# Kernel optimization log

Measured on AMD Instinct MI355X. Metric: run time of the kernel, lower is better.

## Reference

```python
import jax, jax.numpy as jnp
import numpy as np

B, T_ENC, T_DEC = 8, 1024, 100
DMODEL, H, DK, DV, DFF = 512, 8, 64, 64, 2048
L_ENC, L_DEC = 2, 2
EPS = 1e-5
MASK_FILL = -1e10  # original code masked_fills the post-softmax probs with -1e10


def _ln(x, g, b):
    m = jnp.mean(x, -1, keepdims=True)
    v = jnp.mean(jnp.square(x - m), -1, keepdims=True)
    return (x - m) * jax.lax.rsqrt(v + EPS) * g + b


def _mha(Q, K, V, Wq, Wk, Wv, causal):
    Bz, Lq, _ = Q.shape
    Lk = K.shape[1]
    q = (Q @ Wq).reshape(Bz, Lq, H, DK).transpose(0, 2, 1, 3)  # b h q d
    k = (K @ Wk).reshape(Bz, Lk, H, DK).transpose(0, 2, 1, 3)
    v = (V @ Wv).reshape(Bz, Lk, H, DV).transpose(0, 2, 1, 3)
    scores = jnp.einsum('bhqd,bhkd->bhqk', q, k) * (1.0 / np.float32(np.sqrt(DK)))
    p = jax.nn.softmax(scores, axis=-1)
    if causal:
        # faithful to original: mask applied AFTER softmax, fill value -1e10
        mask = jnp.tril(jnp.ones((Lq, Lk), dtype=bool))
        p = jnp.where(mask[None, None], p, jnp.float32(MASK_FILL))
    o = jnp.einsum('bhqk,bhkd->bhqd', p, v)
    return o.transpose(0, 2, 1, 3).reshape(Bz, Lq, H * DV)


def setup_inputs() -> dict:
    key = jax.random.key(0)
    ks = iter(jax.random.split(key, 64))
    s = 0.02
    d = {
        'x': jax.random.normal(next(ks), (B, T_ENC, DMODEL), jnp.float32),
        'y': jax.random.normal(next(ks), (B, T_DEC, DMODEL), jnp.float32),
    }
    def w(shape):
        return jax.random.normal(next(ks), shape, jnp.float32) * s
    # encoder params, stacked over layers
    d['enc_Wq'] = w((L_ENC, DMODEL, DMODEL)); d['enc_Wk'] = w((L_ENC, DMODEL, H * DK))
    d['enc_Wv'] = w((L_ENC, DMODEL, H * DV))
    d['enc_ff_w1'] = w((L_ENC, DMODEL, DFF)); d['enc_ff_b1'] = jnp.zeros((L_ENC, DFF))
    d['enc_ff_w2'] = w((L_ENC, DFF, DMODEL)); d['enc_ff_b2'] = jnp.zeros((L_ENC, DMODEL))
    d['enc_ln1_g'] = jnp.ones((L_ENC, DMODEL)); d['enc_ln1_b'] = jnp.zeros((L_ENC, DMODEL))
    d['enc_ln2_g'] = jnp.ones((L_ENC, DMODEL)); d['enc_ln2_b'] = jnp.zeros((L_ENC, DMODEL))
    # decoder params
    d['dec_Wq1'] = w((L_DEC, DMODEL, DMODEL)); d['dec_Wk1'] = w((L_DEC, DMODEL, H * DK))
    d['dec_Wv1'] = w((L_DEC, DMODEL, H * DV))
    d['dec_Wq2'] = w((L_DEC, DMODEL, DMODEL)); d['dec_Wk2'] = w((L_DEC, DMODEL, H * DK))
    d['dec_Wv2'] = w((L_DEC, DMODEL, H * DV))
    d['dec_ff_w1'] = w((L_DEC, DMODEL, DFF)); d['dec_ff_b1'] = jnp.zeros((L_DEC, DFF))
    d['dec_ff_w2'] = w((L_DEC, DFF, DMODEL)); d['dec_ff_b2'] = jnp.zeros((L_DEC, DMODEL))
    d['dec_ln1_g'] = jnp.ones((L_DEC, DMODEL)); d['dec_ln1_b'] = jnp.zeros((L_DEC, DMODEL))
    d['dec_ln2_g'] = jnp.ones((L_DEC, DMODEL)); d['dec_ln2_b'] = jnp.zeros((L_DEC, DMODEL))
    d['dec_ln3_g'] = jnp.ones((L_DEC, DMODEL)); d['dec_ln3_b'] = jnp.zeros((L_DEC, DMODEL))
    return d


def reference(x, y,
              enc_Wq, enc_Wk, enc_Wv, enc_ff_w1, enc_ff_b1, enc_ff_w2, enc_ff_b2,
              enc_ln1_g, enc_ln1_b, enc_ln2_g, enc_ln2_b,
              dec_Wq1, dec_Wk1, dec_Wv1, dec_Wq2, dec_Wk2, dec_Wv2,
              dec_ff_w1, dec_ff_b1, dec_ff_w2, dec_ff_b2,
              dec_ln1_g, dec_ln1_b, dec_ln2_g, dec_ln2_b, dec_ln3_g, dec_ln3_b):
    # encoder stacks
    for i in range(L_ENC):
        att = _mha(x, x, x, enc_Wq[i], enc_Wk[i], enc_Wv[i], causal=False)
        x1 = _ln(x + att, enc_ln1_g[i], enc_ln1_b[i])
        ff = jax.nn.relu(x1 @ enc_ff_w1[i] + enc_ff_b1[i]) @ enc_ff_w2[i] + enc_ff_b2[i]
        x = _ln(x1 + ff, enc_ln2_g[i], enc_ln2_b[i])
    # decoder stacks
    for i in range(L_DEC):
        a1 = _mha(y, y, y, dec_Wq1[i], dec_Wk1[i], dec_Wv1[i], causal=True)
        y1 = _ln(y + a1, dec_ln1_g[i], dec_ln1_b[i])
        a2 = _mha(y1, x, x, dec_Wq2[i], dec_Wk2[i], dec_Wv2[i], causal=False)
        y2 = _ln(y1 + a2, dec_ln2_g[i], dec_ln2_b[i])
        ff = jax.nn.relu(y2 @ dec_ff_w1[i] + dec_ff_b1[i]) @ dec_ff_w2[i] + dec_ff_b2[i]
        y = _ln(y2 + ff, dec_ln3_g[i], dec_ln3_b[i])
    return y
```

## Files before the change

kernel.cpp:

```cpp
#include <hip/hip_runtime.h>
#include <cstddef>

typedef unsigned short u16;
typedef __attribute__((ext_vector_type(8))) short bf16x8;
typedef __attribute__((ext_vector_type(4))) float f32x4;

__device__ __forceinline__ u16 f2b(float f) {
    union { float f; unsigned u; } x; x.f = f;
    unsigned r = x.u + 0x7FFFu + ((x.u >> 16) & 1u);
    return (u16)(r >> 16);
}
__device__ __forceinline__ float b2f(u16 v) {
    union { unsigned u; float f; } x; x.u = ((unsigned)v) << 16;
    return x.f;
}

__device__ __forceinline__ void gload_lds16(const u16* g, u16* l) {
    __builtin_amdgcn_global_load_lds(
        (const __attribute__((address_space(1))) void*)g,
        (__attribute__((address_space(3))) void*)l, 16, 0, 0);
}

__global__ __launch_bounds__(256) void gemm_mfma_kernel(
    const u16* __restrict__ A, const u16* __restrict__ Bt,
    const float* __restrict__ bias,
    float* __restrict__ Cf, u16* __restrict__ Cb,
    int M, int K, int N, int relu)
{
    __shared__ __align__(16) u16 As[2][128 * 32];
    __shared__ __align__(16) u16 Bs[2][128 * 32];

    const int tid  = threadIdx.x;
    const int wave = tid >> 6;
    const int lane = tid & 63;
    const int m0 = blockIdx.y * 128;
    const int n0 = blockIdx.x * 128;

    const int wm = (wave & 1) * 64;
    const int wn = (wave >> 1) * 64;

    const int srow  = lane >> 2;
    const int skoff = (lane & 3) * 8;

    const int r0 = wave * 32;
    int gr0 = m0 + r0 + srow;       if (gr0 >= M) gr0 = M - 1;
    int gr1 = m0 + r0 + 16 + srow;  if (gr1 >= M) gr1 = M - 1;
    const u16* a0 = A + (size_t)gr0 * K + skoff;
    const u16* a1 = A + (size_t)gr1 * K + skoff;
    const u16* b0p = Bt + (size_t)(n0 + r0 + srow) * K + skoff;
    const u16* b1p = Bt + (size_t)(n0 + r0 + 16 + srow) * K + skoff;

    f32x4 acc[4][4];
#pragma unroll
    for (int i = 0; i < 4; ++i)
#pragma unroll
        for (int j = 0; j < 4; ++j)
            acc[i][j] = (f32x4){0.f, 0.f, 0.f, 0.f};

    const int fm = lane & 15;
    const int fk = (lane >> 4) * 8;

    const int NK = K >> 5;

    gload_lds16(a0, &As[0][(r0) * 32]);
    gload_lds16(a1, &As[0][(r0 + 16) * 32]);
    gload_lds16(b0p, &Bs[0][(r0) * 32]);
    gload_lds16(b1p, &Bs[0][(r0 + 16) * 32]);

    for (int t = 0; t < NK; ++t) {
        const int cur = t & 1;
        __asm__ volatile("s_waitcnt lgkmcnt(0)" ::: "memory");
        __builtin_amdgcn_s_barrier();
        if (t + 1 < NK) {
            const int nxt = (t + 1) & 1;
            const int ko = (t + 1) << 5;
            gload_lds16(a0 + ko, &As[nxt][(r0) * 32]);
            gload_lds16(a1 + ko, &As[nxt][(r0 + 16) * 32]);
            gload_lds16(b0p + ko, &Bs[nxt][(r0) * 32]);
            gload_lds16(b1p + ko, &Bs[nxt][(r0 + 16) * 32]);
            __asm__ volatile("s_waitcnt vmcnt(4)" ::: "memory");
        } else {
            __asm__ volatile("s_waitcnt vmcnt(0)" ::: "memory");
        }
        __builtin_amdgcn_s_barrier();

        bf16x8 af[4], bfr[4];
#pragma unroll
        for (int u = 0; u < 4; ++u) {
            af[u]  = *(const bf16x8*)(&As[cur][(wm + u * 16 + fm) * 32 + fk]);
            bfr[u] = *(const bf16x8*)(&Bs[cur][(wn + u * 16 + fm) * 32 + fk]);
        }
#pragma unroll
        for (int i = 0; i < 4; ++i)
#pragma unroll
            for (int j = 0; j < 4; ++j)
                acc[i][j] = __builtin_amdgcn_mfma_f32_16x16x32_bf16(
                    af[i], bfr[j], acc[i][j], 0, 0, 0);
    }

    const int col = lane & 15;
    const int rq  = (lane >> 4) * 4;
#pragma unroll
    for (int j = 0; j < 4; ++j) {
        const int gn = n0 + wn + j * 16 + col;
        const float bb = bias ? bias[gn] : 0.f;
#pragma unroll
        for (int i = 0; i < 4; ++i) {
            const int gmb = m0 + wm + i * 16 + rq;
#pragma unroll
            for (int r = 0; r < 4; ++r) {
                const int gm = gmb + r;
                if (gm < M) {
                    float v = acc[i][j][r] + bb;
                    if (relu) v = fmaxf(v, 0.f);
                    if (Cb) Cb[(size_t)gm * N + gn] = f2b(v);
                    else    Cf[(size_t)gm * N + gn] = v;
                }
            }
        }
    }
}

__global__ __launch_bounds__(256) void gemm64_kernel(
    const u16* __restrict__ A, const u16* __restrict__ Bt,
    const float* __restrict__ bias,
    float* __restrict__ Cf, u16* __restrict__ Cb,
    int M, int K, int N, int relu)
{
    __shared__ __align__(16) u16 As[2][64 * 32];
    __shared__ __align__(16) u16 Bs[2][64 * 32];

    const int tid  = threadIdx.x;
    const int wave = tid >> 6;
    const int lane = tid & 63;
    const int m0 = blockIdx.y * 64;
    const int n0 = blockIdx.x * 64;
    const int wm = (wave & 1) * 32;
    const int wn = (wave >> 1) * 32;

    const int srow  = lane >> 2;
    const int skoff = (lane & 3) * 8;

    int gr = m0 + wave * 16 + srow; if (gr >= M) gr = M - 1;
    const u16* ap = A + (size_t)gr * K + skoff;
    const u16* bp = Bt + (size_t)(n0 + wave * 16 + srow) * K + skoff;

    f32x4 acc[2][2];
#pragma unroll
    for (int i = 0; i < 2; ++i)
#pragma unroll
        for (int j = 0; j < 2; ++j) acc[i][j] = (f32x4){0.f, 0.f, 0.f, 0.f};

    const int fm = lane & 15;
    const int fk = (lane >> 4) * 8;

    const int NK = K >> 5;

    gload_lds16(ap, &As[0][(wave * 16) * 32]);
    gload_lds16(bp, &Bs[0][(wave * 16) * 32]);

    for (int t = 0; t < NK; ++t) {
        const int cur = t & 1;
        __asm__ volatile("s_waitcnt lgkmcnt(0)" ::: "memory");
        __builtin_amdgcn_s_barrier();
        if (t + 1 < NK) {
            const int nxt = (t + 1) & 1;
            const int ko = (t + 1) << 5;
            gload_lds16(ap + ko, &As[nxt][(wave * 16) * 32]);
            gload_lds16(bp + ko, &Bs[nxt][(wave * 16) * 32]);
            __asm__ volatile("s_waitcnt vmcnt(2)" ::: "memory");
        } else {
            __asm__ volatile("s_waitcnt vmcnt(0)" ::: "memory");
        }
        __builtin_amdgcn_s_barrier();

        bf16x8 af[2], bfr[2];
#pragma unroll
        for (int u = 0; u < 2; ++u) {
            af[u]  = *(const bf16x8*)(&As[cur][(wm + u * 16 + fm) * 32 + fk]);
            bfr[u] = *(const bf16x8*)(&Bs[cur][(wn + u * 16 + fm) * 32 + fk]);
        }
#pragma unroll
        for (int i = 0; i < 2; ++i)
#pragma unroll
            for (int j = 0; j < 2; ++j)
                acc[i][j] = __builtin_amdgcn_mfma_f32_16x16x32_bf16(
                    af[i], bfr[j], acc[i][j], 0, 0, 0);
    }

    const int col = lane & 15;
    const int rq  = (lane >> 4) * 4;
#pragma unroll
    for (int j = 0; j < 2; ++j) {
        const int gn = n0 + wn + j * 16 + col;
        const float bb = bias ? bias[gn] : 0.f;
#pragma unroll
        for (int i = 0; i < 2; ++i) {
            const int gmb = m0 + wm + i * 16 + rq;
#pragma unroll
            for (int r = 0; r < 4; ++r) {
                const int gm = gmb + r;
                if (gm < M) {
                    float v = acc[i][j][r] + bb;
                    if (relu) v = fmaxf(v, 0.f);
                    if (Cb) Cb[(size_t)gm * N + gn] = f2b(v);
                    else    Cf[(size_t)gm * N + gn] = v;
                }
            }
        }
    }
}

__global__ __launch_bounds__(256) void attn_mfma_kernel(
    const u16* __restrict__ Qp, const u16* __restrict__ Kp,
    const u16* __restrict__ Vp, u16* __restrict__ Op,
    int Lq, int Lk, int ldq, int ldkv, int ldo)
{
    const int q0 = blockIdx.x * 128;
    const int h  = blockIdx.y;
    const int b  = blockIdx.z;
    const int tid  = threadIdx.x;
    const int wave = tid >> 6;
    const int lane = tid & 63;
    const int c = lane & 15;
    const int g = lane >> 4;
    const float scale = 0.125f;

    __shared__ __align__(16) u16 Ks[128 * 72];
    __shared__ __align__(16) u16 Vs[64 * 144];
    __shared__ __align__(16) u16 Ps[128 * 144];

    bf16x8 aq[2][2];
#pragma unroll
    for (int half = 0; half < 2; ++half) {
        int qrow = q0 + wave * 32 + half * 16 + c;
        if (qrow > Lq - 1) qrow = Lq - 1;
        const u16* src = Qp + ((size_t)(b * Lq + qrow)) * ldq + h * 64 + g * 8;
        aq[half][0] = *(const bf16x8*)(src);
        aq[half][1] = *(const bf16x8*)(src + 32);
    }

    float den[2][4] = {};
    f32x4 o[2][4];
#pragma unroll
    for (int half = 0; half < 2; ++half)
#pragma unroll
        for (int j = 0; j < 4; ++j) o[half][j] = (f32x4){0.f, 0.f, 0.f, 0.f};

    const int srow = tid & 63;
    const int sseg = tid >> 6;

    for (int t = 0; t < (Lk >> 7); ++t) {
        const int k0 = t << 7;
        __syncthreads();
#pragma unroll
        for (int sub = 0; sub < 2; ++sub) {
            const int kr = k0 + sub * 64 + srow;
            const u16* kg = Kp + ((size_t)(b * Lk + kr)) * ldkv + h * 64;
            *(bf16x8*)(&Ks[(sub * 64 + srow) * 72 + sseg * 8])      = *(const bf16x8*)(kg + sseg * 8);
            *(bf16x8*)(&Ks[(sub * 64 + srow) * 72 + 32 + sseg * 8]) = *(const bf16x8*)(kg + 32 + sseg * 8);
            const u16* vg = Vp + ((size_t)(b * Lk + kr)) * ldkv + h * 64;
            bf16x8 v0 = *(const bf16x8*)(vg + sseg * 8);
            bf16x8 v1 = *(const bf16x8*)(vg + 32 + sseg * 8);
#pragma unroll
            for (int i = 0; i < 8; ++i) {
                Vs[(sseg * 8 + i) * 144 + sub * 64 + srow]      = (u16)v0[i];
                Vs[(32 + sseg * 8 + i) * 144 + sub * 64 + srow] = (u16)v1[i];
            }
        }
        __syncthreads();

#pragma unroll
        for (int half = 0; half < 2; ++half) {
            f32x4 s[8];
#pragma unroll
            for (int jn = 0; jn < 8; ++jn) s[jn] = (f32x4){0.f, 0.f, 0.f, 0.f};
#pragma unroll
            for (int jn = 0; jn < 8; ++jn) {
                bf16x8 b0 = *(const bf16x8*)(&Ks[(jn * 16 + c) * 72 + g * 8]);
                bf16x8 b1 = *(const bf16x8*)(&Ks[(jn * 16 + c) * 72 + 32 + g * 8]);
                s[jn] = __builtin_amdgcn_mfma_f32_16x16x32_bf16(aq[half][0], b0, s[jn], 0, 0, 0);
                s[jn] = __builtin_amdgcn_mfma_f32_16x16x32_bf16(aq[half][1], b1, s[jn], 0, 0, 0);
            }
#pragma unroll
            for (int jn = 0; jn < 8; ++jn)
#pragma unroll
                for (int r = 0; r < 4; ++r) {
                    const float p = __expf(s[jn][r] * scale);
                    den[half][r] += p;
                    Ps[(wave * 32 + half * 16 + g * 4 + r) * 144 + jn * 16 + c] = f2b(p);
                }
        }

        __asm__ volatile("s_waitcnt lgkmcnt(0)" ::: "memory");

#pragma unroll
        for (int half = 0; half < 2; ++half) {
            const int qr = (wave * 32 + half * 16 + c) * 144;
#pragma unroll
            for (int sub = 0; sub < 2; ++sub) {
                bf16x8 ap0 = *(const bf16x8*)(&Ps[qr + sub * 64 + g * 8]);
                bf16x8 ap1 = *(const bf16x8*)(&Ps[qr + sub * 64 + 32 + g * 8]);
#pragma unroll
                for (int jd = 0; jd < 4; ++jd) {
                    bf16x8 b0 = *(const bf16x8*)(&Vs[(jd * 16 + c) * 144 + sub * 64 + g * 8]);
                    bf16x8 b1 = *(const bf16x8*)(&Vs[(jd * 16 + c) * 144 + sub * 64 + 32 + g * 8]);
                    o[half][jd] = __builtin_amdgcn_mfma_f32_16x16x32_bf16(ap0, b0, o[half][jd], 0, 0, 0);
                    o[half][jd] = __builtin_amdgcn_mfma_f32_16x16x32_bf16(ap1, b1, o[half][jd], 0, 0, 0);
                }
            }
        }
    }

#pragma unroll
    for (int half = 0; half < 2; ++half)
#pragma unroll
        for (int r = 0; r < 4; ++r) {
#pragma unroll
            for (int msk = 1; msk < 16; msk <<= 1)
                den[half][r] += __shfl_xor(den[half][r], msk, 64);
        }

#pragma unroll
    for (int half = 0; half < 2; ++half)
#pragma unroll
        for (int r = 0; r < 4; ++r) {
            const int q = q0 + wave * 32 + half * 16 + g * 4 + r;
            if (q < Lq) {
                const float inv = 1.0f / den[half][r];
#pragma unroll
                for (int jd = 0; jd < 4; ++jd)
                    Op[((size_t)(b * Lq + q)) * ldo + h * 64 + jd * 16 + c] =
                        f2b(o[half][jd][r] * inv);
            }
        }
}

__global__ __launch_bounds__(256) void attn_causal_kernel(
    const u16* __restrict__ Qp, const u16* __restrict__ Kp,
    const u16* __restrict__ Vp, const float* __restrict__ SuffV,
    u16* __restrict__ Op,
    int Lq, int Lk, int ldq, int ldkv, int ldo)
{
    const int q0 = blockIdx.x * 128;
    const int h  = blockIdx.y;
    const int b  = blockIdx.z;
    const int tid  = threadIdx.x;
    const int wave = tid >> 6;
    const int lane = tid & 63;
    const int c = lane & 15;
    const int g = lane >> 4;
    const float scale = 0.125f;

    __shared__ __align__(16) u16 Ks[64 * 72];
    __shared__ __align__(16) u16 Vs[64 * 72];
    __shared__ __align__(16) u16 Ps[128 * 72];

    bf16x8 aq[2][2];
#pragma unroll
    for (int half = 0; half < 2; ++half) {
        int qrow = q0 + wave * 32 + half * 16 + c;
        if (qrow > Lq - 1) qrow = Lq - 1;
        const u16* src = Qp + ((size_t)(b * Lq + qrow)) * ldq + h * 64 + g * 8;
        aq[half][0] = *(const bf16x8*)(src);
        aq[half][1] = *(const bf16x8*)(src + 32);
    }

    float den[2][4] = {};
    f32x4 o[2][4];
#pragma unroll
    for (int half = 0; half < 2; ++half)
#pragma unroll
        for (int j = 0; j < 4; ++j) o[half][j] = (f32x4){0.f, 0.f, 0.f, 0.f};

    const int srow = tid & 63;
    const int sseg = tid >> 6;
    const int ntiles = (Lk + 63) >> 6;

    for (int t = 0; t < ntiles; ++t) {
        const int k0 = t << 6;
        __syncthreads();
        {
            int kr = k0 + srow; if (kr > Lk - 1) kr = Lk - 1;
            const u16* kg = Kp + ((size_t)(b * Lk + kr)) * ldkv + h * 64;
            *(bf16x8*)(&Ks[srow * 72 + sseg * 8])      = *(const bf16x8*)(kg + sseg * 8);
            *(bf16x8*)(&Ks[srow * 72 + 32 + sseg * 8]) = *(const bf16x8*)(kg + 32 + sseg * 8);
            const u16* vg = Vp + ((size_t)(b * Lk + kr)) * ldkv + h * 64;
            bf16x8 v0 = *(const bf16x8*)(vg + sseg * 8);
            bf16x8 v1 = *(const bf16x8*)(vg + 32 + sseg * 8);
#pragma unroll
            for (int i = 0; i < 8; ++i) {
                Vs[(sseg * 8 + i) * 72 + srow]      = (u16)v0[i];
                Vs[(32 + sseg * 8 + i) * 72 + srow] = (u16)v1[i];
            }
        }
        __syncthreads();

#pragma unroll
        for (int half = 0; half < 2; ++half) {
            f32x4 s[4];
#pragma unroll
            for (int jn = 0; jn < 4; ++jn) s[jn] = (f32x4){0.f, 0.f, 0.f, 0.f};
#pragma unroll
            for (int jn = 0; jn < 4; ++jn) {
                bf16x8 b0 = *(const bf16x8*)(&Ks[(jn * 16 + c) * 72 + g * 8]);
                bf16x8 b1 = *(const bf16x8*)(&Ks[(jn * 16 + c) * 72 + 32 + g * 8]);
                s[jn] = __builtin_amdgcn_mfma_f32_16x16x32_bf16(aq[half][0], b0, s[jn], 0, 0, 0);
                s[jn] = __builtin_amdgcn_mfma_f32_16x16x32_bf16(aq[half][1], b1, s[jn], 0, 0, 0);
            }
#pragma unroll
            for (int jn = 0; jn < 4; ++jn)
#pragma unroll
                for (int r = 0; r < 4; ++r) {
                    const int kcol = k0 + jn * 16 + c;
                    const int qrow = q0 + wave * 32 + half * 16 + g * 4 + r;
                    const float e = __expf(s[jn][r] * scale);
                    const float ev = (kcol < Lk) ? e : 0.f;
                    den[half][r] += ev;
                    const float pv = (kcol <= qrow) ? ev : 0.f;
                    Ps[(wave * 32 + half * 16 + g * 4 + r) * 72 + jn * 16 + c] = f2b(pv);
                }
        }

        __asm__ volatile("s_waitcnt lgkmcnt(0)" ::: "memory");

#pragma unroll
        for (int half = 0; half < 2; ++half) {
            bf16x8 ap0 = *(const bf16x8*)(&Ps[(wave * 32 + half * 16 + c) * 72 + g * 8]);
            bf16x8 ap1 = *(const bf16x8*)(&Ps[(wave * 32 + half * 16 + c) * 72 + 32 + g * 8]);
#pragma unroll
            for (int jd = 0; jd < 4; ++jd) {
                bf16x8 b0 = *(const bf16x8*)(&Vs[(jd * 16 + c) * 72 + g * 8]);
                bf16x8 b1 = *(const bf16x8*)(&Vs[(jd * 16 + c) * 72 + 32 + g * 8]);
                o[half][jd] = __builtin_amdgcn_mfma_f32_16x16x32_bf16(ap0, b0, o[half][jd], 0, 0, 0);
                o[half][jd] = __builtin_amdgcn_mfma_f32_16x16x32_bf16(ap1, b1, o[half][jd], 0, 0, 0);
            }
        }
    }

#pragma unroll
    for (int half = 0; half < 2; ++half)
#pragma unroll
        for (int r = 0; r < 4; ++r) {
#pragma unroll
            for (int msk = 1; msk < 16; msk <<= 1)
                den[half][r] += __shfl_xor(den[half][r], msk, 64);
        }

#pragma unroll
    for (int half = 0; half < 2; ++half)
#pragma unroll
        for (int r = 0; r < 4; ++r) {
            const int q = q0 + wave * 32 + half * 16 + g * 4 + r;
            if (q < Lq) {
                const float inv = 1.0f / den[half][r];
                const float* sv = SuffV + ((size_t)(b * Lq + q)) * 512 + h * 64;
#pragma unroll
                for (int jd = 0; jd < 4; ++jd)
                    Op[((size_t)(b * Lq + q)) * ldo + h * 64 + jd * 16 + c] =
                        f2b(o[half][jd][r] * inv - 1.0e10f * sv[jd * 16 + c]);
            }
        }
}

__global__ __launch_bounds__(64) void suffv_kernel(
    const u16* __restrict__ Vp, float* __restrict__ SuffV, int Lq, int ldv)
{
    const int b = blockIdx.x;
    const int h = blockIdx.y;
    const int d = threadIdx.x;
    float acc = 0.f;
    for (int q = Lq - 1; q >= 0; --q) {
        SuffV[((size_t)(b * Lq + q)) * 512 + h * 64 + d] = acc;
        acc += b2f(Vp[((size_t)(b * Lq + q)) * ldv + h * 64 + d]);
    }
}

__global__ __launch_bounds__(256) void attn_split_kernel(
    const u16* __restrict__ Qp, const u16* __restrict__ Kp,
    const u16* __restrict__ Vp, float* __restrict__ Opart,
    float* __restrict__ Dpart,
    int Lq, int Lk, int ldq, int ldkv, int nsplit)
{
    const int q0 = blockIdx.x * 64;
    const int h  = blockIdx.y;
    const int b  = blockIdx.z / nsplit;
    const int sp = blockIdx.z % nsplit;
    const int tid  = threadIdx.x;
    const int wave = tid >> 6;
    const int lane = tid & 63;
    const int c = lane & 15;
    const int g = lane >> 4;
    const float scale = 0.125f;
    const int rowsTot = gridDim.z / nsplit * Lq;

    __shared__ __align__(16) u16 Ks[64 * 72];
    __shared__ __align__(16) u16 Vs[64 * 72];
    __shared__ __align__(16) u16 Ps[64 * 72];

    bf16x8 aq[2];
    {
        int qrow = q0 + wave * 16 + c;
        if (qrow > Lq - 1) qrow = Lq - 1;
        const u16* src = Qp + ((size_t)(b * Lq + qrow)) * ldq + h * 64 + g * 8;
        aq[0] = *(const bf16x8*)(src);
        aq[1] = *(const bf16x8*)(src + 32);
    }

    float den[4] = {0.f, 0.f, 0.f, 0.f};
    f32x4 o[4];
#pragma unroll
    for (int j = 0; j < 4; ++j) o[j] = (f32x4){0.f, 0.f, 0.f, 0.f};

    const int srow = tid & 63;
    const int sseg = tid >> 6;
    const int ntile = (Lk >> 6) / nsplit;

    for (int t = sp * ntile; t < (sp + 1) * ntile; ++t) {
        const int k0 = t << 6;
        __syncthreads();
        {
            const u16* kg = Kp + ((size_t)(b * Lk + k0 + srow)) * ldkv + h * 64;
            *(bf16x8*)(&Ks[srow * 72 + sseg * 8])      = *(const bf16x8*)(kg + sseg * 8);
            *(bf16x8*)(&Ks[srow * 72 + 32 + sseg * 8]) = *(const bf16x8*)(kg + 32 + sseg * 8);
            const u16* vg = Vp + ((size_t)(b * Lk + k0 + srow)) * ldkv + h * 64;
            bf16x8 v0 = *(const bf16x8*)(vg + sseg * 8);
            bf16x8 v1 = *(const bf16x8*)(vg + 32 + sseg * 8);
#pragma unroll
            for (int i = 0; i < 8; ++i) {
                Vs[(sseg * 8 + i) * 72 + srow]      = (u16)v0[i];
                Vs[(32 + sseg * 8 + i) * 72 + srow] = (u16)v1[i];
            }
        }
        __syncthreads();

        f32x4 s[4];
#pragma unroll
        for (int jn = 0; jn < 4; ++jn) s[jn] = (f32x4){0.f, 0.f, 0.f, 0.f};
#pragma unroll
        for (int jn = 0; jn < 4; ++jn) {
            bf16x8 b0 = *(const bf16x8*)(&Ks[(jn * 16 + c) * 72 + g * 8]);
            bf16x8 b1 = *(const bf16x8*)(&Ks[(jn * 16 + c) * 72 + 32 + g * 8]);
            s[jn] = __builtin_amdgcn_mfma_f32_16x16x32_bf16(aq[0], b0, s[jn], 0, 0, 0);
            s[jn] = __builtin_amdgcn_mfma_f32_16x16x32_bf16(aq[1], b1, s[jn], 0, 0, 0);
        }
#pragma unroll
        for (int jn = 0; jn < 4; ++jn)
#pragma unroll
            for (int r = 0; r < 4; ++r) {
                const float p = __expf(s[jn][r] * scale);
                den[r] += p;
                Ps[(wave * 16 + g * 4 + r) * 72 + jn * 16 + c] = f2b(p);
            }

        __asm__ volatile("s_waitcnt lgkmcnt(0)" ::: "memory");

        bf16x8 ap0 = *(const bf16x8*)(&Ps[(wave * 16 + c) * 72 + g * 8]);
        bf16x8 ap1 = *(const bf16x8*)(&Ps[(wave * 16 + c) * 72 + 32 + g * 8]);
#pragma unroll
        for (int jd = 0; jd < 4; ++jd) {
            bf16x8 b0 = *(const bf16x8*)(&Vs[(jd * 16 + c) * 72 + g * 8]);
            bf16x8 b1 = *(const bf16x8*)(&Vs[(jd * 16 + c) * 72 + 32 + g * 8]);
            o[jd] = __builtin_amdgcn_mfma_f32_16x16x32_bf16(ap0, b0, o[jd], 0, 0, 0);
            o[jd] = __builtin_amdgcn_mfma_f32_16x16x32_bf16(ap1, b1, o[jd], 0, 0, 0);
        }
    }

#pragma unroll
    for (int r = 0; r < 4; ++r) {
#pragma unroll
        for (int msk = 1; msk < 16; msk <<= 1)
            den[r] += __shfl_xor(den[r], msk, 64);
    }

#pragma unroll
    for (int r = 0; r < 4; ++r) {
        const int q = q0 + wave * 16 + g * 4 + r;
        if (q < Lq) {
            const size_t prow = (size_t)sp * rowsTot + b * Lq + q;
#pragma unroll
            for (int jd = 0; jd < 4; ++jd)
                Opart[prow * 512 + h * 64 + jd * 16 + c] = o[jd][r];
            if (c == 0) Dpart[prow * 8 + h] = den[r];
        }
    }
}

__global__ __launch_bounds__(256) void combine_ln_kernel(
    const float* __restrict__ Opart, const float* __restrict__ Dpart,
    int nsplit, int nrows,
    const float* __restrict__ R,
    const float* __restrict__ g, const float* __restrict__ beta,
    float* __restrict__ O, u16* __restrict__ Ob)
{
    const int row = blockIdx.x * 4 + (threadIdx.x >> 6);
    const int lane = threadIdx.x & 63;
    if (row >= nrows) return;
    const size_t base = (size_t)row * 512 + lane * 8;
    const int h = lane >> 3;

    float sd = 0.f;
    float v[8] = {};
    for (int s = 0; s < nsplit; ++s) {
        sd += Dpart[((size_t)s * nrows + row) * 8 + h];
        const float* op = Opart + ((size_t)s * nrows + row) * 512 + lane * 8;
        float4 a = *(const float4*)(op);
        float4 b = *(const float4*)(op + 4);
        v[0] += a.x; v[1] += a.y; v[2] += a.z; v[3] += a.w;
        v[4] += b.x; v[5] += b.y; v[6] += b.z; v[7] += b.w;
    }
    const float invd = 1.0f / sd;
    {
        float4 a = *(const float4*)(R + base);
        float4 b = *(const float4*)(R + base + 4);
        v[0] = v[0] * invd + a.x; v[1] = v[1] * invd + a.y;
        v[2] = v[2] * invd + a.z; v[3] = v[3] * invd + a.w;
        v[4] = v[4] * invd + b.x; v[5] = v[5] * invd + b.y;
        v[6] = v[6] * invd + b.z; v[7] = v[7] * invd + b.w;
    }

    float sum = 0.f;
#pragma unroll
    for (int i = 0; i < 8; ++i) sum += v[i];
#pragma unroll
    for (int msk = 1; msk < 64; msk <<= 1) sum += __shfl_xor(sum, msk, 64);
    const float mean = sum * (1.0f / 512.0f);

    float var = 0.f;
#pragma unroll
    for (int i = 0; i < 8; ++i) { v[i] -= mean; var += v[i] * v[i]; }
#pragma unroll
    for (int msk = 1; msk < 64; msk <<= 1) var += __shfl_xor(var, msk, 64);
    const float rstd = rsqrtf(var * (1.0f / 512.0f) + 1e-5f);

    float o[8];
#pragma unroll
    for (int i = 0; i < 8; ++i)
        o[i] = v[i] * rstd * g[lane * 8 + i] + beta[lane * 8 + i];

    *(float4*)(O + base)     = make_float4(o[0], o[1], o[2], o[3]);
    *(float4*)(O + base + 4) = make_float4(o[4], o[5], o[6], o[7]);
    if (Ob) {
        bf16x8 ob;
#pragma unroll
        for (int i = 0; i < 8; ++i) ob[i] = (short)f2b(o[i]);
        *(bf16x8*)(Ob + base) = ob;
    }
}

struct WT9 { const float* src[9]; unsigned dst[9]; unsigned os[9]; };
struct WT4 { const float* src[4]; unsigned dst[4]; int K[4]; int N[4]; };

__device__ __forceinline__ void wtrans_tile(
    const float* Wl, u16* Wtl, int K, int N, int k0, int n0, int tid)
{
    __shared__ float t[32][33];
    const int tr = tid >> 3;
    const int tc = (tid & 7) * 4;
    float4 v = *(const float4*)(Wl + (size_t)(k0 + tr) * N + n0 + tc);
    t[tr][tc] = v.x; t[tr][tc + 1] = v.y; t[tr][tc + 2] = v.z; t[tr][tc + 3] = v.w;
    __syncthreads();
    ushort4 o;
    o.x = f2b(t[tc + 0][tr]); o.y = f2b(t[tc + 1][tr]);
    o.z = f2b(t[tc + 2][tr]); o.w = f2b(t[tc + 3][tr]);
    *(ushort4*)(Wtl + (size_t)(n0 + tr) * K + k0 + tc) = o;
}

__global__ __launch_bounds__(256) void wtrans9_kernel(WT9 d, u16* __restrict__ WB)
{
    const int w = blockIdx.z >> 1;
    const int layer = blockIdx.z & 1;
    const float* Wl = d.src[w] + (size_t)layer * 512 * 512;
    u16* Wtl = WB + d.dst[w] + (size_t)layer * d.os[w];
    wtrans_tile(Wl, Wtl, 512, 512, blockIdx.y * 32, blockIdx.x * 32, threadIdx.x);
}

__global__ __launch_bounds__(256) void wtrans4_kernel(WT4 d, u16* __restrict__ WB)
{
    const int w = blockIdx.z >> 1;
    const int layer = blockIdx.z & 1;
    const int K = d.K[w], N = d.N[w];
    const int k0 = blockIdx.y * 32, n0 = blockIdx.x * 32;
    if (k0 >= K || n0 >= N) return;
    const float* Wl = d.src[w] + (size_t)layer * K * N;
    u16* Wtl = WB + d.dst[w] + (size_t)layer * 1048576;
    wtrans_tile(Wl, Wtl, K, N, k0, n0, threadIdx.x);
}

__global__ __launch_bounds__(256) void conv2_kernel(
    const float* __restrict__ X0, u16* __restrict__ Y0, int n0,
    const float* __restrict__ X1, u16* __restrict__ Y1, int n1)
{
    int i = (blockIdx.x * 256 + threadIdx.x) * 8;
    const float* X; u16* Y;
    if (i < n0) { X = X0 + i; Y = Y0 + i; }
    else if (i < n0 + n1) { X = X1 + (i - n0); Y = Y1 + (i - n0); }
    else return;
    float4 a = *(const float4*)(X);
    float4 b = *(const float4*)(X + 4);
    ushort4 o0, o1;
    o0.x = f2b(a.x); o0.y = f2b(a.y); o0.z = f2b(a.z); o0.w = f2b(a.w);
    o1.x = f2b(b.x); o1.y = f2b(b.y); o1.z = f2b(b.z); o1.w = f2b(b.w);
    *(ushort4*)(Y) = o0;
    *(ushort4*)(Y + 4) = o1;
}

__global__ __launch_bounds__(256) void ln_kernel(
    const float* __restrict__ Xf, const u16* __restrict__ Xb,
    const float* __restrict__ R,
    const float* __restrict__ g, const float* __restrict__ beta,
    float* __restrict__ O, u16* __restrict__ Ob, int nrows)
{
    const int row = blockIdx.x * 4 + (threadIdx.x >> 6);
    const int lane = threadIdx.x & 63;
    if (row >= nrows) return;
    const size_t base = (size_t)row * 512 + lane * 8;

    float v[8];
    if (Xf) {
        float4 a = *(const float4*)(Xf + base);
        float4 b = *(const float4*)(Xf + base + 4);
        v[0] = a.x; v[1] = a.y; v[2] = a.z; v[3] = a.w;
        v[4] = b.x; v[5] = b.y; v[6] = b.z; v[7] = b.w;
    } else {
        bf16x8 xb = *(const bf16x8*)(Xb + base);
#pragma unroll
        for (int i = 0; i < 8; ++i) v[i] = b2f((u16)xb[i]);
    }
    {
        float4 a = *(const float4*)(R + base);
        float4 b = *(const float4*)(R + base + 4);
        v[0] += a.x; v[1] += a.y; v[2] += a.z; v[3] += a.w;
        v[4] += b.x; v[5] += b.y; v[6] += b.z; v[7] += b.w;
    }

    float sum = 0.f;
#pragma unroll
    for (int i = 0; i < 8; ++i) sum += v[i];
#pragma unroll
    for (int msk = 1; msk < 64; msk <<= 1) sum += __shfl_xor(sum, msk, 64);
    const float mean = sum * (1.0f / 512.0f);

    float var = 0.f;
#pragma unroll
    for (int i = 0; i < 8; ++i) { v[i] -= mean; var += v[i] * v[i]; }
#pragma unroll
    for (int msk = 1; msk < 64; msk <<= 1) var += __shfl_xor(var, msk, 64);
    const float rstd = rsqrtf(var * (1.0f / 512.0f) + 1e-5f);

    float o[8];
#pragma unroll
    for (int i = 0; i < 8; ++i)
        o[i] = v[i] * rstd * g[lane * 8 + i] + beta[lane * 8 + i];

    *(float4*)(O + base)     = make_float4(o[0], o[1], o[2], o[3]);
    *(float4*)(O + base + 4) = make_float4(o[4], o[5], o[6], o[7]);
    if (Ob) {
        bf16x8 ob;
#pragma unroll
        for (int i = 0; i < 8; ++i) ob[i] = (short)f2b(o[i]);
        *(bf16x8*)(Ob + base) = ob;
    }
}

extern "C" void kernel_launch(void* const* d_in, const int* in_sizes, int n_in,
                              void* d_out, int out_size, void* d_ws, size_t ws_size,
                              hipStream_t stream)
{
    const int B = 8, T_ENC = 1024, T_DEC = 100, DM = 512, DFF = 2048;
    const int ME = B * T_ENC;
    const int MD = B * T_DEC;
    const int L = 2;
    const int NSPLIT = 4;

    int idx = 0;
    const float* x0    = (const float*)d_in[idx++];
    const float* y0    = (const float*)d_in[idx++];
    const float* eWq   = (const float*)d_in[idx++];
    const float* eWk   = (const float*)d_in[idx++];
    const float* eWv   = (const float*)d_in[idx++];
    const float* eW1   = (const float*)d_in[idx++];
    const float* eB1   = (const float*)d_in[idx++];
    const float* eW2   = (const float*)d_in[idx++];
    const float* eB2   = (const float*)d_in[idx++];
    const float* eLn1g = (const float*)d_in[idx++];
    const float* eLn1b = (const float*)d_in[idx++];
    const float* eLn2g = (const float*)d_in[idx++];
    const float* eLn2b = (const float*)d_in[idx++];
    const float* dWq1  = (const float*)d_in[idx++];
    const float* dWk1  = (const float*)d_in[idx++];
    const float* dWv1  = (const float*)d_in[idx++];
    const float* dWq2  = (const float*)d_in[idx++];
    const float* dWk2  = (const float*)d_in[idx++];
    const float* dWv2  = (const float*)d_in[idx++];
    const float* dW1   = (const float*)d_in[idx++];
    const float* dB1   = (const float*)d_in[idx++];
    const float* dW2   = (const float*)d_in[idx++];
    const float* dB2   = (const float*)d_in[idx++];
    const float* dLn1g = (const float*)d_in[idx++];
    const float* dLn1b = (const float*)d_in[idx++];
    const float* dLn2g = (const float*)d_in[idx++];
    const float* dLn2b = (const float*)d_in[idx++];
    const float* dLn3g = (const float*)d_in[idx++];
    const float* dLn3b = (const float*)d_in[idx++];

    float* ws = (float*)d_ws;
    u16* OV    = (u16*)ws;
    u16* QKVb  = OV;
    u16* H1b   = OV;
    u16* CKVb  = OV;
    u16* AFb    = (u16*)(ws + 8388608);
    float* Dpart = ws + 8388608;
    float* X1   = ws + 10485760;
    float* XOUT = ws + 14680064;
    float* SuffV = ws + 18874368;
    float* Opart = ws + 18874368;
    float* DA    = ws + 20103168;
    float* Y1   = ws + 20512768;
    float* Y2   = ws + 20922368;
    float* YOUT = ws + 21331968;
    u16* ub  = (u16*)(ws + 21741568);
    u16* XBc = ub;
    u16* YB  = ub + 4194304;
    u16* Y1b = ub + 4603904;
    u16* Y2b = ub + 5013504;
    u16* DQb = ub + 5423104;
    u16* DAb = ub + 5832704;
    u16* DHb = ub + 6242304;
    u16* DQKVb = DHb;
    u16* WB  = ub + 7880704;

    const unsigned eQKVT = 0, eW1T = 1572864, eW2T = 3670016,
                   dQKV1T = 5767168, dWq2T = 7340032, dKV2T = 7864320,
                   dW1T = 8912896, dW2T = 11010048;

    auto gemm = [&](const u16* A, const u16* Bt, const float* bias, float* Cf, u16* Cb,
                    int M, int K, int N, int relu) {
        dim3 grid(N / 128, (M + 127) / 128);
        hipLaunchKernelGGL(gemm_mfma_kernel, grid, dim3(256), 0, stream,
                           A, Bt, bias, Cf, Cb, M, K, N, relu);
    };
    auto gemm64 = [&](const u16* A, const u16* Bt, const float* bias, float* Cf, u16* Cb,
                      int M, int K, int N, int relu) {
        dim3 grid(N / 64, (M + 63) / 64);
        hipLaunchKernelGGL(gemm64_kernel, grid, dim3(256), 0, stream,
                           A, Bt, bias, Cf, Cb, M, K, N, relu);
    };
    auto ln = [&](const float* Xf, const u16* Xb, const float* R, const float* g,
                  const float* bta, float* O, u16* Ob, int rows) {
        hipLaunchKernelGGL(ln_kernel, dim3((rows + 3) / 4), dim3(256), 0, stream,
                           Xf, Xb, R, g, bta, O, Ob, rows);
    };

    {
        WT9 w9;
        const float* s9[9] = {eWq, eWk, eWv, dWq1, dWk1, dWv1, dWq2, dWk2, dWv2};
        const unsigned d9[9] = {eQKVT, eQKVT + 262144, eQKVT + 524288,
                                dQKV1T, dQKV1T + 262144, dQKV1T + 524288,
                                dWq2T, dKV2T, dKV2T + 262144};
        const unsigned o9[9] = {786432, 786432, 786432, 786432, 786432, 786432,
                                262144, 524288, 524288};
        for (int i = 0; i < 9; ++i) { w9.src[i] = s9[i]; w9.dst[i] = d9[i]; w9.os[i] = o9[i]; }
        hipLaunchKernelGGL(wtrans9_kernel, dim3(16, 16, 18), dim3(256), 0, stream, w9, WB);

        WT4 w4;
        const float* s4[4] = {eW1, eW2, dW1, dW2};
        const unsigned d4[4] = {eW1T, eW2T, dW1T, dW2T};
        const int K4[4] = {512, 2048, 512, 2048};
        const int N4[4] = {2048, 512, 2048, 512};
        for (int i = 0; i < 4; ++i) { w4.src[i] = s4[i]; w4.dst[i] = d4[i]; w4.K[i] = K4[i]; w4.N[i] = N4[i]; }
        hipLaunchKernelGGL(wtrans4_kernel, dim3(64, 64, 8), dim3(256), 0, stream, w4, WB);

        const int n0 = ME * DM, n1 = MD * DM;
        hipLaunchKernelGGL(conv2_kernel, dim3((n0 + n1) / 8 / 256), dim3(256), 0, stream,
                           x0, XBc, n0, y0, YB, n1);
    }

    const int BS = DM;
    const int B1S = DFF;

    const float* xin = x0;
    for (int i = 0; i < L; ++i) {
        gemm(XBc, WB + eQKVT + (size_t)i * 786432, nullptr, nullptr, QKVb, ME, DM, 1536, 0);
        {
            dim3 grid(T_ENC / 128, 8, B);
            hipLaunchKernelGGL(attn_mfma_kernel, grid, dim3(256), 0, stream,
                               QKVb, QKVb + 512, QKVb + 1024, AFb,
                               T_ENC, T_ENC, 1536, 1536, 512);
        }
        ln(nullptr, AFb, xin, eLn1g + i * BS, eLn1b + i * BS, X1, XBc, ME);
        gemm(XBc, WB + eW1T + (size_t)i * 1048576, eB1 + i * B1S, nullptr, H1b, ME, DM, DFF, 1);
        gemm(H1b, WB + eW2T + (size_t)i * 1048576, eB2 + i * BS, nullptr, AFb, ME, DFF, DM, 0);
        ln(nullptr, AFb, X1, eLn2g + i * BS, eLn2b + i * BS, XOUT, XBc, ME);
        xin = XOUT;
    }

    gemm(XBc, WB + dKV2T, nullptr, nullptr, CKVb, ME, DM, 2048, 0);

    const float* yin = y0;
    for (int i = 0; i < L; ++i) {
        gemm64(YB, WB + dQKV1T + (size_t)i * 786432, nullptr, nullptr, DQKVb, MD, DM, 1536, 0);
        hipLaunchKernelGGL(suffv_kernel, dim3(B, 8), dim3(64), 0, stream,
                           DQKVb + 1024, SuffV, T_DEC, 1536);
        {
            dim3 grid((T_DEC + 127) / 128, 8, B);
            hipLaunchKernelGGL(attn_causal_kernel, grid, dim3(256), 0, stream,
                               DQKVb, DQKVb + 512, DQKVb + 1024, SuffV, DAb,
                               T_DEC, T_DEC, 1536, 1536, 512);
        }
        ln(nullptr, DAb, yin, dLn1g + i * BS, dLn1b + i * BS, Y1, Y1b, MD);
        gemm64(Y1b, WB + dWq2T + (size_t)i * 262144, nullptr, nullptr, DQb, MD, DM, DM, 0);
        {
            dim3 grid((T_DEC + 63) / 64, 8, B * NSPLIT);
            hipLaunchKernelGGL(attn_split_kernel, grid, dim3(256), 0, stream,
                               DQb, CKVb + (size_t)i * 1024, CKVb + (size_t)i * 1024 + 512,
                               Opart, Dpart, T_DEC, T_ENC, 512, 2048, NSPLIT);
            hipLaunchKernelGGL(combine_ln_kernel, dim3((MD + 3) / 4), dim3(256), 0, stream,
                               Opart, Dpart, NSPLIT, MD,
                               Y1, dLn2g + i * BS, dLn2b + i * BS, Y2, Y2b);
        }
        gemm64(Y2b, WB + dW1T + (size_t)i * 1048576, dB1 + i * B1S, nullptr, DHb, MD, DM, DFF, 1);
        gemm64(DHb, WB + dW2T + (size_t)i * 1048576, dB2 + i * BS, DA, nullptr, MD, DFF, DM, 0);
        float* yout = (i == L - 1) ? (float*)d_out : YOUT;
        ln(DA, nullptr, Y2, dLn3g + i * BS, dLn3b + i * BS, yout,
           (i == L - 1) ? nullptr : YB, MD);
        yin = yout;
    }
}
```

Baseline: 830.7 us.

## Prefetch next K/V tile into registers and repad LDS rows to avoid bank conflicts

The encoder attention kernel now loads the next 128-key K/V tile from global memory into registers while the current tile is computed. At the top of each iteration it stores those registers to LDS, so global load latency overlaps the MFMA work. The row strides of the V and P tiles in LDS are also changed (144→148, 72→76) in three attention kernels to cut bank conflicts on the transposed V stores and on the P scatter writes. The cost is extra VGPRs for the prefetch buffers, which may lower occupancy, plus slightly more LDS.

```diff
diff --git a/kernel.cpp b/kernel.cpp
--- a/kernel.cpp
+++ b/kernel.cpp
@@ -227,8 +227,8 @@
     const float scale = 0.125f;
 
     __shared__ __align__(16) u16 Ks[128 * 72];
-    __shared__ __align__(16) u16 Vs[64 * 144];
-    __shared__ __align__(16) u16 Ps[128 * 144];
+    __shared__ __align__(16) u16 Vs[64 * 148];
+    __shared__ __align__(16) u16 Ps[128 * 148];
 
     bf16x8 aq[2][2];
 #pragma unroll
@@ -250,25 +250,43 @@
     const int srow = tid & 63;
     const int sseg = tid >> 6;
 
-    for (int t = 0; t < (Lk >> 7); ++t) {
-        const int k0 = t << 7;
-        __syncthreads();
+    bf16x8 kreg[2][4], vreg[2][4];
+    auto loadKV = [&](int t, int s) {
 #pragma unroll
         for (int sub = 0; sub < 2; ++sub) {
-            const int kr = k0 + sub * 64 + srow;
+            const int kr = (t << 7) + sub * 64 + srow;
             const u16* kg = Kp + ((size_t)(b * Lk + kr)) * ldkv + h * 64;
-            *(bf16x8*)(&Ks[(sub * 64 + srow) * 72 + sseg * 8])      = *(const bf16x8*)(kg + sseg * 8);
-            *(bf16x8*)(&Ks[(sub * 64 + srow) * 72 + 32 + sseg * 8]) = *(const bf16x8*)(kg + 32 + sseg * 8);
+            kreg[s][sub * 2 + 0] = *(const bf16x8*)(kg + sseg * 8);
+            kreg[s][sub * 2 + 1] = *(const bf16x8*)(kg + 32 + sseg * 8);
             const u16* vg = Vp + ((size_t)(b * Lk + kr)) * ldkv + h * 64;
-            bf16x8 v0 = *(const bf16x8*)(vg + sseg * 8);
-            bf16x8 v1 = *(const bf16x8*)(vg + 32 + sseg * 8);
+            vreg[s][sub * 2 + 0] = *(const bf16x8*)(vg + sseg * 8);
+            vreg[s][sub * 2 + 1] = *(const bf16x8*)(vg + 32 + sseg * 8);
+        }
+    };
+    auto storeKV = [&](int s) {
+#pragma unroll
+        for (int sub = 0; sub < 2; ++sub) {
+            *(bf16x8*)(&Ks[(sub * 64 + srow) * 72 + sseg * 8])      = kreg[s][sub * 2 + 0];
+            *(bf16x8*)(&Ks[(sub * 64 + srow) * 72 + 32 + sseg * 8]) = kreg[s][sub * 2 + 1];
 #pragma unroll
             for (int i = 0; i < 8; ++i) {
-                Vs[(sseg * 8 + i) * 144 + sub * 64 + srow]      = (u16)v0[i];
-                Vs[(32 + sseg * 8 + i) * 144 + sub * 64 + srow] = (u16)v1[i];
-            }
-        }
-        __syncthreads();
+                Vs[(sseg * 8 + i) * 148 + sub * 64 + srow]      = (u16)vreg[s][sub * 2 + 0][i];
+                Vs[(32 + sseg * 8 + i) * 148 + sub * 64 + srow] = (u16)vreg[s][sub * 2 + 1][i];
+            }
+        }
+    };
+
+    const int nt = Lk >> 7;
+    loadKV(0, 0);
+
+    for (int t = 0; t < nt; ++t) {
+        const int cur = t & 1;
+        __asm__ volatile("s_waitcnt lgkmcnt(0)" ::: "memory");
+        __builtin_amdgcn_s_barrier();
+        storeKV(cur);
+        if (t + 1 < nt) loadKV(t + 1, cur ^ 1);
+        __asm__ volatile("s_waitcnt lgkmcnt(0)" ::: "memory");
+        __builtin_amdgcn_s_barrier();
 
 #pragma unroll
         for (int half = 0; half < 2; ++half) {
@@ -288,7 +306,7 @@
                 for (int r = 0; r < 4; ++r) {
                     const float p = __expf(s[jn][r] * scale);
                     den[half][r] += p;
-                    Ps[(wave * 32 + half * 16 + g * 4 + r) * 144 + jn * 16 + c] = f2b(p);
+                    Ps[(wave * 32 + half * 16 + g * 4 + r) * 148 + jn * 16 + c] = f2b(p);
                 }
         }
 
@@ -296,15 +314,15 @@
 
 #pragma unroll
         for (int half = 0; half < 2; ++half) {
-            const int qr = (wave * 32 + half * 16 + c) * 144;
+            const int qr = (wave * 32 + half * 16 + c) * 148;
 #pragma unroll
             for (int sub = 0; sub < 2; ++sub) {
                 bf16x8 ap0 = *(const bf16x8*)(&Ps[qr + sub * 64 + g * 8]);
                 bf16x8 ap1 = *(const bf16x8*)(&Ps[qr + sub * 64 + 32 + g * 8]);
 #pragma unroll
                 for (int jd = 0; jd < 4; ++jd) {
-                    bf16x8 b0 = *(const bf16x8*)(&Vs[(jd * 16 + c) * 144 + sub * 64 + g * 8]);
-                    bf16x8 b1 = *(const bf16x8*)(&Vs[(jd * 16 + c) * 144 + sub * 64 + 32 + g * 8]);
+                    bf16x8 b0 = *(const bf16x8*)(&Vs[(jd * 16 + c) * 148 + sub * 64 + g * 8]);
+                    bf16x8 b1 = *(const bf16x8*)(&Vs[(jd * 16 + c) * 148 + sub * 64 + 32 + g * 8]);
                     o[half][jd] = __builtin_amdgcn_mfma_f32_16x16x32_bf16(ap0, b0, o[half][jd], 0, 0, 0);
                     o[half][jd] = __builtin_amdgcn_mfma_f32_16x16x32_bf16(ap1, b1, o[half][jd], 0, 0, 0);
                 }
@@ -354,7 +372,7 @@
 
     __shared__ __align__(16) u16 Ks[64 * 72];
     __shared__ __align__(16) u16 Vs[64 * 72];
-    __shared__ __align__(16) u16 Ps[128 * 72];
+    __shared__ __align__(16) u16 Ps[128 * 76];
 
     bf16x8 aq[2][2];
 #pragma unroll
@@ -418,7 +436,7 @@
                     const float ev = (kcol < Lk) ? e : 0.f;
                     den[half][r] += ev;
                     const float pv = (kcol <= qrow) ? ev : 0.f;
-                    Ps[(wave * 32 + half * 16 + g * 4 + r) * 72 + jn * 16 + c] = f2b(pv);
+                    Ps[(wave * 32 + half * 16 + g * 4 + r) * 76 + jn * 16 + c] = f2b(pv);
                 }
         }
 
@@ -426,8 +444,8 @@
 
 #pragma unroll
         for (int half = 0; half < 2; ++half) {
-            bf16x8 ap0 = *(const bf16x8*)(&Ps[(wave * 32 + half * 16 + c) * 72 + g * 8]);
-            bf16x8 ap1 = *(const bf16x8*)(&Ps[(wave * 32 + half * 16 + c) * 72 + 32 + g * 8]);
+            bf16x8 ap0 = *(const bf16x8*)(&Ps[(wave * 32 + half * 16 + c) * 76 + g * 8]);
+            bf16x8 ap1 = *(const bf16x8*)(&Ps[(wave * 32 + half * 16 + c) * 76 + 32 + g * 8]);
 #pragma unroll
             for (int jd = 0; jd < 4; ++jd) {
                 bf16x8 b0 = *(const bf16x8*)(&Vs[(jd * 16 + c) * 72 + g * 8]);
@@ -496,7 +514,7 @@
 
     __shared__ __align__(16) u16 Ks[64 * 72];
     __shared__ __align__(16) u16 Vs[64 * 72];
-    __shared__ __align__(16) u16 Ps[64 * 72];
+    __shared__ __align__(16) u16 Ps[64 * 76];
 
     bf16x8 aq[2];
     {
@@ -550,13 +568,13 @@
             for (int r = 0; r < 4; ++r) {
                 const float p = __expf(s[jn][r] * scale);
                 den[r] += p;
-                Ps[(wave * 16 + g * 4 + r) * 72 + jn * 16 + c] = f2b(p);
+                Ps[(wave * 16 + g * 4 + r) * 76 + jn * 16 + c] = f2b(p);
             }
 
         __asm__ volatile("s_waitcnt lgkmcnt(0)" ::: "memory");
 
-        bf16x8 ap0 = *(const bf16x8*)(&Ps[(wave * 16 + c) * 72 + g * 8]);
-        bf16x8 ap1 = *(const bf16x8*)(&Ps[(wave * 16 + c) * 72 + 32 + g * 8]);
+        bf16x8 ap0 = *(const bf16x8*)(&Ps[(wave * 16 + c) * 76 + g * 8]);
+        bf16x8 ap1 = *(const bf16x8*)(&Ps[(wave * 16 + c) * 76 + 32 + g * 8]);
 #pragma unroll
         for (int jd = 0; jd < 4; ++jd) {
             bf16x8 b0 = *(const bf16x8*)(&Vs[(jd * 16 + c) * 72 + g * 8]);
```

Measured after the change: 2.762 ms. 3.32x slower.
